# Kernel optimization log

Measured on AMD Instinct MI355X. Metric: run time of the kernel, lower is better.

Reference implementation:

```python
import jax, jax.numpy as jnp
import numpy as np

N = 100000
E = 3200000
IN_DIM = 256
HID = 64
NC = 32
K1 = 2  # conv1 propagation steps
EPS = 1e-5


def setup_inputs() -> dict:
    key = jax.random.key(0)
    ks = jax.random.split(key, 8)
    x = jax.random.normal(ks[0], (N, IN_DIM), dtype=jnp.float32)
    src = jax.random.randint(ks[1], (E,), 0, N)
    dst = jax.random.randint(ks[2], (E,), 0, N)
    W1 = jax.random.normal(ks[3], (IN_DIM, HID), dtype=jnp.float32) / np.sqrt(IN_DIM)
    b1 = jnp.zeros((HID,), dtype=jnp.float32)
    gamma = jnp.ones((HID,), dtype=jnp.float32)
    beta = jnp.zeros((HID,), dtype=jnp.float32)
    W2 = jax.random.normal(ks[4], (HID, NC), dtype=jnp.float32) / np.sqrt(HID)
    b2 = jnp.zeros((NC,), dtype=jnp.float32)
    return {"x": x, "src": src, "dst": dst, "W1": W1, "b1": b1,
            "gamma": gamma, "beta": beta, "W2": W2, "b2": b2}


def _gcn_norm(src, dst, n):
    # deg includes self loop (add_self_loops=True): deg[i] = 1 + in-degree
    deg = jax.ops.segment_sum(jnp.ones_like(src, dtype=jnp.float32), dst, num_segments=n) + 1.0
    dinv = jax.lax.rsqrt(deg)
    w_edge = dinv[src] * dinv[dst]      # [E] normalized edge weights
    w_self = dinv * dinv                # [N] self-loop weights (1/deg)
    return w_edge, w_self


def _propagate(h, src, dst, w_edge, w_self, n):
    # out = D^-1/2 (A+I) D^-1/2 h  via gather-scale-scatter
    msg = w_edge[:, None] * h[src]
    agg = jax.ops.segment_sum(msg, dst, num_segments=n)
    return agg + w_self[:, None] * h


def reference(x, src, dst, W1, b1, gamma, beta, W2, b2):
    n = x.shape[0]
    w_edge, w_self = _gcn_norm(src, dst, n)
    # conv1: K-step propagation then linear
    h = x
    for _ in range(K1):
        h = _propagate(h, src, dst, w_edge, w_self, n)
    h = h @ W1 + b1
    # batchnorm (training-mode batch stats over nodes, biased variance)
    mean = jnp.mean(h, axis=0)
    var = jnp.mean(jnp.square(h - mean), axis=0)
    h = (h - mean) * jax.lax.rsqrt(var + EPS) * gamma + beta
    h = jax.nn.selu(h)
    # dropout p=0.0 -> identity
    # conv2: 1-step propagation then linear
    h = _propagate(h, src, dst, w_edge, w_self, n)
    h = h @ W2 + b2
    return jax.nn.log_softmax(h, axis=1)
```

## Files before the change

kernel.cpp:

```cpp
#include <hip/hip_runtime.h>
#include <hip/hip_fp16.h>

#define NN 100000
#define EE 3200000
#define NB 256
#define NPB 391
#define BCAP 13568
#define NBLK_A 512
#define CHUNK_A (EE / NBLK_A)

#define OFF_AF   0UL
#define OFF_AH   25600000UL
#define OFF_BH   38400000UL
#define OFF_CNT  (OFF_BH + 65536UL)
#define OFF_LOC  (OFF_CNT + 524288UL)
#define OFF_P    (OFF_LOC + 524288UL)
#define OFF_CSR  51200000UL
#define OFF_RP   64000000UL
#define OFF_DINV 64400384UL
#define OFF_SEG  64800768UL
#define OFF_BASE 64808960UL
#define OFF_BN   64813056UL
#define OFF_SS   64813568UL

typedef __attribute__((ext_vector_type(8))) short bf16x8;
typedef __attribute__((ext_vector_type(4))) float f32x4;

__global__ __launch_bounds__(256) void passA2(const int* __restrict__ src, const int* __restrict__ dst,
                                              int* __restrict__ cnt, int* __restrict__ loc,
                                              unsigned* __restrict__ gbuf) {
    __shared__ unsigned ebuf[CHUNK_A];
    __shared__ int hist[NB], cur[NB], sc[NB];
    int t = threadIdx.x, b = blockIdx.x;
    hist[t] = 0;
    __syncthreads();
    int beg = b * CHUNK_A;
    for (int i = t; i < CHUNK_A; i += 256)
        atomicAdd(&hist[dst[beg + i] / NPB], 1);
    __syncthreads();
    int h = hist[t];
    sc[t] = h;
    __syncthreads();
    for (int off = 1; off < 256; off <<= 1) {
        int v = (t >= off) ? sc[t - off] : 0;
        __syncthreads();
        sc[t] += v;
        __syncthreads();
    }
    int ex = sc[t] - h;
    cur[t] = ex;
    loc[b * NB + t] = ex;
    cnt[b * NB + t] = h;
    __syncthreads();
    for (int i = t; i < CHUNK_A; i += 256) {
        int d = dst[beg + i];
        int k = d / NPB;
        int dl = d - k * NPB;
        int p = atomicAdd(&cur[k], 1);
        ebuf[p] = ((unsigned)dl << 17) | (unsigned)src[beg + i];
    }
    __syncthreads();
    for (int i = t; i < CHUNK_A; i += 256)
        gbuf[beg + i] = ebuf[i];
}

__global__ __launch_bounds__(512) void colscan(const int* __restrict__ cnt, int* __restrict__ P,
                                               int* __restrict__ total) {
    __shared__ int s[512];
    int k = blockIdx.x, t = threadIdx.x;
    int v = cnt[t * NB + k];
    s[t] = v;
    __syncthreads();
    for (int off = 1; off < 512; off <<= 1) {
        int u = (t >= off) ? s[t - off] : 0;
        __syncthreads();
        s[t] += u;
        __syncthreads();
    }
    P[t * NB + k] = s[t] - v;
    if (t == 511) total[k] = s[511];
}

__global__ __launch_bounds__(256) void basescan(const int* __restrict__ total, int* __restrict__ base,
                                                int* __restrict__ rp) {
    __shared__ int s[256];
    int t = threadIdx.x;
    int v = total[t];
    s[t] = v;
    __syncthreads();
    for (int off = 1; off < 256; off <<= 1) {
        int u = (t >= off) ? s[t - off] : 0;
        __syncthreads();
        s[t] += u;
        __syncthreads();
    }
    base[t] = s[t] - v;
    if (t == 255) { base[256] = s[255]; rp[NN] = s[255]; }
}

__global__ __launch_bounds__(512) void passB2(const unsigned* __restrict__ gbuf,
                                              const int* __restrict__ cnt, const int* __restrict__ loc,
                                              const int* __restrict__ P, const int* __restrict__ total,
                                              const int* __restrict__ base,
                                              int* __restrict__ rp, float* __restrict__ dinv,
                                              int* __restrict__ csr) {
    __shared__ unsigned ebuf[BCAP];
    __shared__ int deg_l[NPB];
    __shared__ int off_l[NPB];
    __shared__ int s[512];
    int k = blockIdx.x, t = threadIdx.x;
    int nb = min(total[k], BCAP);
    for (int i = t; i < NPB; i += 512) deg_l[i] = 0;
    int wid = t >> 6, lane = t & 63;
    for (int b = wid; b < NBLK_A; b += 8) {
        int n = cnt[b * NB + k];
        int so = b * CHUNK_A + loc[b * NB + k];
        int dofs = P[b * NB + k];
        for (int e = lane; e < n; e += 64)
            if (dofs + e < BCAP) ebuf[dofs + e] = gbuf[so + e];
    }
    __syncthreads();
    for (int j = t; j < nb; j += 512) atomicAdd(&deg_l[ebuf[j] >> 17], 1);
    __syncthreads();
    int d0 = (t < NPB) ? deg_l[t] : 0;
    s[t] = d0;
    __syncthreads();
    for (int off = 1; off < 512; off <<= 1) {
        int v = (t >= off) ? s[t - off] : 0;
        __syncthreads();
        s[t] += v;
        __syncthreads();
    }
    if (t < NPB) off_l[t] = s[t] - d0;
    __syncthreads();
    int nodebase = k * NPB;
    int cbase = base[k];
    for (int i = t; i < NPB; i += 512) {
        int node = nodebase + i;
        if (node < NN) {
            rp[node] = cbase + off_l[i];
            dinv[node] = rsqrtf((float)deg_l[i] + 1.0f);
        }
    }
    __syncthreads();
    for (int j = t; j < nb; j += 512) {
        unsigned e = ebuf[j];
        int p = atomicAdd(&off_l[e >> 17], 1);
        csr[cbase + p] = (int)(e & 0x1FFFFu);
    }
}

__global__ __launch_bounds__(256) void wprep(const float* __restrict__ W1, short* __restrict__ wf) {
    int e = blockIdx.x * 256 + threadIdx.x;
    if (e >= 16384) return;
    int j = e & 7, lane = (e >> 3) & 63, nt = (e >> 9) & 3, ks = e >> 11;
    int k = ks * 32 + (lane >> 4) * 8 + j;
    int col = nt * 16 + (lane & 15);
    float w = W1[k * 64 + col];
    unsigned b = __float_as_uint(w);
    short hi = (short)(b >> 16);
    float hf = __uint_as_float(b & 0xFFFF0000u);
    float lo = w - hf;
    short lov = (short)(__float_as_uint(lo) >> 16);
    wf[((size_t)(ks * 8 + nt * 2 + 0) * 64 + lane) * 8 + j] = hi;
    wf[((size_t)(ks * 8 + nt * 2 + 1) * 64 + lane) * 8 + j] = lov;
}

__global__ __launch_bounds__(256) void gemm1(const float* __restrict__ x, const short* __restrict__ wf,
                                             const float* __restrict__ dinv, __half* __restrict__ Ah) {
    int wid = threadIdx.x >> 6, lane = threadIdx.x & 63;
    int g = blockIdx.x * 4 + wid;
    if (g >= NN / 16) return;
    int lrow = g * 16 + (lane & 15);
    int kgrp = (lane >> 4) * 8;
    const float* xp = x + (size_t)lrow * 256 + kgrp;
    f32x4 acc[4];
    #pragma unroll
    for (int nt = 0; nt < 4; ++nt) acc[nt] = (f32x4){0.f, 0.f, 0.f, 0.f};
    for (int ks = 0; ks < 8; ++ks) {
        float4 f0 = *(const float4*)(xp + ks * 32);
        float4 f1 = *(const float4*)(xp + ks * 32 + 4);
        bf16x8 a_hi, a_lo;
        const float* fp = &f0.x;
        #pragma unroll
        for (int j = 0; j < 8; ++j) {
            float f = (j < 4) ? fp[j] : (&f1.x)[j - 4];
            unsigned b = __float_as_uint(f);
            a_hi[j] = (short)(b >> 16);
            float lo = f - __uint_as_float(b & 0xFFFF0000u);
            a_lo[j] = (short)(__float_as_uint(lo) >> 16);
        }
        const short* wfk = wf + (size_t)(ks * 8) * 64 * 8;
        #pragma unroll
        for (int nt = 0; nt < 4; ++nt) {
            bf16x8 b_hi = *(const bf16x8*)(wfk + ((nt * 2 + 0) * 64 + lane) * 8);
            bf16x8 b_lo = *(const bf16x8*)(wfk + ((nt * 2 + 1) * 64 + lane) * 8);
            acc[nt] = __builtin_amdgcn_mfma_f32_16x16x32_bf16(a_hi, b_hi, acc[nt], 0, 0, 0);
            acc[nt] = __builtin_amdgcn_mfma_f32_16x16x32_bf16(a_hi, b_lo, acc[nt], 0, 0, 0);
            acc[nt] = __builtin_amdgcn_mfma_f32_16x16x32_bf16(a_lo, b_hi, acc[nt], 0, 0, 0);
        }
    }
    int mb = (lane >> 4) * 4;
    #pragma unroll
    for (int reg = 0; reg < 4; ++reg) {
        int row = g * 16 + mb + reg;
        float dv = dinv[row];
        #pragma unroll
        for (int nt = 0; nt < 4; ++nt)
            Ah[(size_t)row * 64 + nt * 16 + (lane & 15)] = __float2half(acc[nt][reg] * dv);
    }
}

template <int P>
__global__ __launch_bounds__(256) void agg64h(const __half* __restrict__ h, __half* __restrict__ outp,
                                              const int* __restrict__ rp, const int* __restrict__ csr,
                                              const float* __restrict__ dinv) {
    int lane = threadIdx.x & 63;
    int node = (blockIdx.x << 2) + (threadIdx.x >> 6);
    if (node >= NN) return;
    int hid = lane >> 5;
    int c2 = (lane & 31) * 2;
    float dd = dinv[node];
    float ax = 0.f, ay = 0.f, bx = 0.f, by = 0.f;
    if (hid == 0) {
        __half2 sv = *(const __half2*)(h + (size_t)node * 64 + c2);
        ax = __half2float(sv.x); ay = __half2float(sv.y);
    }
    int beg = rp[node], end = rp[node + 1];
    for (int j0 = beg; j0 < end; j0 += 64) {
        int m = end - j0; if (m > 64) m = 64;
        int s = csr[j0 + (lane < m ? lane : 0)];
        int j = 0;
        for (; j + 15 < m; j += 16) {
            int i0 = __shfl(s, j + hid);
            int i1 = __shfl(s, j + 2 + hid);
            int i2 = __shfl(s, j + 4 + hid);
            int i3 = __shfl(s, j + 6 + hid);
            int i4 = __shfl(s, j + 8 + hid);
            int i5 = __shfl(s, j + 10 + hid);
            int i6 = __shfl(s, j + 12 + hid);
            int i7 = __shfl(s, j + 14 + hid);
            __half2 v0 = *(const __half2*)(h + (size_t)i0 * 64 + c2);
            __half2 v1 = *(const __half2*)(h + (size_t)i1 * 64 + c2);
            __half2 v2 = *(const __half2*)(h + (size_t)i2 * 64 + c2);
            __half2 v3 = *(const __half2*)(h + (size_t)i3 * 64 + c2);
            __half2 v4 = *(const __half2*)(h + (size_t)i4 * 64 + c2);
            __half2 v5 = *(const __half2*)(h + (size_t)i5 * 64 + c2);
            __half2 v6 = *(const __half2*)(h + (size_t)i6 * 64 + c2);
            __half2 v7 = *(const __half2*)(h + (size_t)i7 * 64 + c2);
            ax += __half2float(v0.x) + __half2float(v2.x);
            ay += __half2float(v0.y) + __half2float(v2.y);
            bx += __half2float(v1.x) + __half2float(v3.x);
            by += __half2float(v1.y) + __half2float(v3.y);
            ax += __half2float(v4.x) + __half2float(v6.x);
            ay += __half2float(v4.y) + __half2float(v6.y);
            bx += __half2float(v5.x) + __half2float(v7.x);
            by += __half2float(v5.y) + __half2float(v7.y);
        }
        for (; j + 7 < m; j += 8) {
            int i0 = __shfl(s, j + hid);
            int i1 = __shfl(s, j + 2 + hid);
            int i2 = __shfl(s, j + 4 + hid);
            int i3 = __shfl(s, j + 6 + hid);
            __half2 v0 = *(const __half2*)(h + (size_t)i0 * 64 + c2);
            __half2 v1 = *(const __half2*)(h + (size_t)i1 * 64 + c2);
            __half2 v2 = *(const __half2*)(h + (size_t)i2 * 64 + c2);
            __half2 v3 = *(const __half2*)(h + (size_t)i3 * 64 + c2);
            ax += __half2float(v0.x) + __half2float(v2.x);
            ay += __half2float(v0.y) + __half2float(v2.y);
            bx += __half2float(v1.x) + __half2float(v3.x);
            by += __half2float(v1.y) + __half2float(v3.y);
        }
        for (; j < m; j += 2) {
            int idx = j + hid;
            int cidx = idx < m ? idx : m - 1;
            int sj = __shfl(s, cidx);
            if (idx < m) {
                __half2 v = *(const __half2*)(h + (size_t)sj * 64 + c2);
                ax += __half2float(v.x); ay += __half2float(v.y);
            }
        }
    }
    float sx = ax + bx, sy = ay + by;
    sx += __shfl(sx, lane ^ 32);
    sy += __shfl(sy, lane ^ 32);
    if (hid == 0) {
        float w = (P == 2) ? dd * dd : dd;
        __half2 o;
        o.x = __float2half(sx * w); o.y = __float2half(sy * w);
        *(__half2*)(outp + (size_t)node * 64 + c2) = o;
    }
}

__global__ __launch_bounds__(256) void agg32f(const __half* __restrict__ U, float* __restrict__ outp,
                                              const int* __restrict__ rp, const int* __restrict__ csr,
                                              const float* __restrict__ dinv, const float* __restrict__ b2) {
    int lane = threadIdx.x & 63;
    int node = (blockIdx.x << 2) + (threadIdx.x >> 6);
    if (node >= NN) return;
    int gid = lane >> 4;
    int c2 = (lane & 15) * 2;
    float dd = dinv[node];
    float ax = 0.f, ay = 0.f;
    if (gid == 0) {
        __half2 sv = *(const __half2*)(U + (size_t)node * 32 + c2);
        ax = __half2float(sv.x); ay = __half2float(sv.y);
    }
    int beg = rp[node], end = rp[node + 1];
    for (int j0 = beg; j0 < end; j0 += 64) {
        int m = end - j0; if (m > 64) m = 64;
        int s = csr[j0 + (lane < m ? lane : 0)];
        int j = 0;
        for (; j + 15 < m; j += 16) {
            int i0 = __shfl(s, j + gid);
            int i1 = __shfl(s, j + 4 + gid);
            int i2 = __shfl(s, j + 8 + gid);
            int i3 = __shfl(s, j + 12 + gid);
            __half2 v0 = *(const __half2*)(U + (size_t)i0 * 32 + c2);
            __half2 v1 = *(const __half2*)(U + (size_t)i1 * 32 + c2);
            __half2 v2 = *(const __half2*)(U + (size_t)i2 * 32 + c2);
            __half2 v3 = *(const __half2*)(U + (size_t)i3 * 32 + c2);
            ax += __half2float(v0.x) + __half2float(v1.x) + __half2float(v2.x) + __half2float(v3.x);
            ay += __half2float(v0.y) + __half2float(v1.y) + __half2float(v2.y) + __half2float(v3.y);
        }
        for (; j + 7 < m; j += 8) {
            int i0 = __shfl(s, j + gid);
            int i1 = __shfl(s, j + 4 + gid);
            __half2 v0 = *(const __half2*)(U + (size_t)i0 * 32 + c2);
            __half2 v1 = *(const __half2*)(U + (size_t)i1 * 32 + c2);
            ax += __half2float(v0.x) + __half2float(v1.x);
            ay += __half2float(v0.y) + __half2float(v1.y);
        }
        for (; j < m; j += 4) {
            int idx = j + gid;
            int cidx = idx < m ? idx : m - 1;
            int sj = __shfl(s, cidx);
            if (idx < m) {
                __half2 v = *(const __half2*)(U + (size_t)sj * 32 + c2);
                ax += __half2float(v.x); ay += __half2float(v.y);
            }
        }
    }
    ax += __shfl(ax, lane ^ 16); ay += __shfl(ay, lane ^ 16);
    ax += __shfl(ax, lane ^ 32); ay += __shfl(ay, lane ^ 32);
    float v0 = ax * dd + b2[c2];
    float v1 = ay * dd + b2[c2 + 1];
    float mx = fmaxf(v0, v1);
    mx = fmaxf(mx, __shfl_xor(mx, 1));
    mx = fmaxf(mx, __shfl_xor(mx, 2));
    mx = fmaxf(mx, __shfl_xor(mx, 4));
    mx = fmaxf(mx, __shfl_xor(mx, 8));
    float sum = __expf(v0 - mx) + __expf(v1 - mx);
    sum += __shfl_xor(sum, 1);
    sum += __shfl_xor(sum, 2);
    sum += __shfl_xor(sum, 4);
    sum += __shfl_xor(sum, 8);
    if (gid == 0) {
        float ls = __logf(sum);
        *(float2*)(outp + (size_t)node * 32 + c2) = make_float2(v0 - mx - ls, v1 - mx - ls);
    }
}

__global__ __launch_bounds__(256) void bn_stats(const __half* __restrict__ A, float* __restrict__ bn) {
    int t = threadIdx.x;
    int c = t & 63, rg = t >> 6;
    float s = 0.f, sq = 0.f;
    for (int r = blockIdx.x * 4 + rg; r < NN; r += gridDim.x * 4) {
        float v = __half2float(A[(size_t)r * 64 + c]);
        s += v; sq += v * v;
    }
    __shared__ float ls[256], lq[256];
    ls[t] = s; lq[t] = sq;
    __syncthreads();
    if (t < 64) {
        float S = ls[t] + ls[t + 64] + ls[t + 128] + ls[t + 192];
        float Q = lq[t] + lq[t + 64] + lq[t + 128] + lq[t + 192];
        atomicAdd(&bn[t], S);
        atomicAdd(&bn[64 + t], Q);
    }
}

__global__ void bn_final(const float* __restrict__ bn, const float* __restrict__ gamma,
                         const float* __restrict__ beta, float* __restrict__ ss) {
    int c = threadIdx.x;
    float mean = bn[c] / (float)NN;
    float var = bn[64 + c] / (float)NN - mean * mean;
    float sc = gamma[c] * rsqrtf(var + 1e-5f);
    ss[c] = sc;
    ss[64 + c] = beta[c] - mean * sc;
}

__global__ __launch_bounds__(256) void gemm2(const __half* __restrict__ A, const float* __restrict__ W2,
                                             const float* __restrict__ ss, const float* __restrict__ dinv,
                                             __half* __restrict__ U) {
    __shared__ float w2s[64 * 32];
    __shared__ float sc[64], sh[64];
    for (int i = threadIdx.x; i < 512; i += 256)
        ((float4*)w2s)[i] = ((const float4*)W2)[i];
    if (threadIdx.x < 64) {
        sc[threadIdx.x] = ss[threadIdx.x];
        sh[threadIdx.x] = ss[64 + threadIdx.x];
    }
    __syncthreads();
    const float SELU_S = 1.0507009873554805f;
    const float SELU_AS = 1.7580993408473766f;
    int lane = threadIdx.x & 31, grp = threadIdx.x >> 5;
    int node = blockIdx.x * 8 + grp;
    if (node >= NN) return;
    const __half* Ar = A + (size_t)node * 64;
    float v0 = __half2float(Ar[lane]);
    float v1 = __half2float(Ar[lane + 32]);
    v0 = v0 * sc[lane] + sh[lane];
    v1 = v1 * sc[lane + 32] + sh[lane + 32];
    v0 = v0 > 0.f ? SELU_S * v0 : SELU_AS * (__expf(v0) - 1.0f);
    v1 = v1 > 0.f ? SELU_S * v1 : SELU_AS * (__expf(v1) - 1.0f);
    float acc = 0.f;
    #pragma unroll
    for (int j = 0; j < 32; ++j) {
        acc += __shfl(v0, j, 32) * w2s[j * 32 + lane];
        acc += __shfl(v1, j, 32) * w2s[(j + 32) * 32 + lane];
    }
    U[(size_t)node * 32 + lane] = __float2half(dinv[node] * acc);
}

extern "C" void kernel_launch(void* const* d_in, const int* in_sizes, int n_in,
                              void* d_out, int out_size, void* d_ws, size_t ws_size,
                              hipStream_t stream) {
    const float* x     = (const float*)d_in[0];
    const int*   src   = (const int*)d_in[1];
    const int*   dst   = (const int*)d_in[2];
    const float* W1    = (const float*)d_in[3];
    const float* gamma = (const float*)d_in[5];
    const float* beta  = (const float*)d_in[6];
    const float* W2    = (const float*)d_in[7];
    const float* b2    = (const float*)d_in[8];
    float* out = (float*)d_out;

    char* ws = (char*)d_ws;
    __half*   Af   = (__half*)(ws + OFF_AF);
    unsigned* gbuf = (unsigned*)(ws + OFF_AF);
    __half*   Ah   = (__half*)(ws + OFF_AH);
    __half*   Bh   = (__half*)(ws + OFF_BH);
    short*    wf   = (short*)(ws + OFF_BH);
    __half*   Uh   = (__half*)(ws + OFF_BH);
    int*      cnt  = (int*)(ws + OFF_CNT);
    int*      loc  = (int*)(ws + OFF_LOC);
    int*      Pm   = (int*)(ws + OFF_P);
    int*      csr  = (int*)(ws + OFF_CSR);
    int*      rp   = (int*)(ws + OFF_RP);
    float*    dinv = (float*)(ws + OFF_DINV);
    int*      tot  = (int*)(ws + OFF_SEG);
    int*      base = (int*)(ws + OFF_BASE);
    float*    bn   = (float*)(ws + OFF_BN);
    float*    ssb  = (float*)(ws + OFF_SS);

    hipMemsetAsync(bn, 0, 128 * sizeof(float), stream);

    wprep<<<64, 256, 0, stream>>>(W1, wf);

    passA2<<<NBLK_A, 256, 0, stream>>>(src, dst, cnt, loc, gbuf);
    colscan<<<NB, 512, 0, stream>>>(cnt, Pm, tot);
    basescan<<<1, 256, 0, stream>>>(tot, base, rp);
    passB2<<<NB, 512, 0, stream>>>(gbuf, cnt, loc, Pm, tot, base, rp, dinv, csr);

    gemm1<<<(NN / 16 + 3) / 4, 256, 0, stream>>>(x, wf, dinv, Ah);
    agg64h<2><<<NN / 4, 256, 0, stream>>>(Ah, Bh, rp, csr, dinv);
    agg64h<1><<<NN / 4, 256, 0, stream>>>(Bh, Af, rp, csr, dinv);

    bn_stats<<<1024, 256, 0, stream>>>(Af, bn);
    bn_final<<<1, 64, 0, stream>>>(bn, gamma, beta, ssb);

    gemm2<<<NN / 8, 256, 0, stream>>>(Af, W2, ssb, dinv, Uh);
    agg32f<<<NN / 4, 256, 0, stream>>>(Uh, out, rp, csr, dinv, b2);
}
```

Before: 388.7 us.

## Drop column scan and LDS staging in CSR build; read gbuf per-thread directly

Removes the colscan kernel and computes per-bucket totals inside basescan by summing 512 counts per thread. passB2 no longer stages bucket edges into shared memory; each of the 512 threads walks its own source block's segment of gbuf serially, twice (degree count, then scatter). This saves a launch and the LDS capacity limit, but basescan becomes a long serial loop in a single block, and the per-thread serial reads of gbuf are uncoalesced and read twice.

```diff
diff --git a/kernel.cpp b/kernel.cpp
--- a/kernel.cpp
+++ b/kernel.cpp
@@ -5,7 +5,6 @@
 #define EE 3200000
 #define NB 256
 #define NPB 391
-#define BCAP 13568
 #define NBLK_A 512
 #define CHUNK_A (EE / NBLK_A)
 
@@ -14,11 +13,9 @@
 #define OFF_BH   38400000UL
 #define OFF_CNT  (OFF_BH + 65536UL)
 #define OFF_LOC  (OFF_CNT + 524288UL)
-#define OFF_P    (OFF_LOC + 524288UL)
 #define OFF_CSR  51200000UL
 #define OFF_RP   64000000UL
 #define OFF_DINV 64400384UL
-#define OFF_SEG  64800768UL
 #define OFF_BASE 64808960UL
 #define OFF_BN   64813056UL
 #define OFF_SS   64813568UL
@@ -64,28 +61,12 @@
         gbuf[beg + i] = ebuf[i];
 }
 
-__global__ __launch_bounds__(512) void colscan(const int* __restrict__ cnt, int* __restrict__ P,
-                                               int* __restrict__ total) {
-    __shared__ int s[512];
-    int k = blockIdx.x, t = threadIdx.x;
-    int v = cnt[t * NB + k];
-    s[t] = v;
-    __syncthreads();
-    for (int off = 1; off < 512; off <<= 1) {
-        int u = (t >= off) ? s[t - off] : 0;
-        __syncthreads();
-        s[t] += u;
-        __syncthreads();
-    }
-    P[t * NB + k] = s[t] - v;
-    if (t == 511) total[k] = s[511];
-}
-
-__global__ __launch_bounds__(256) void basescan(const int* __restrict__ total, int* __restrict__ base,
+__global__ __launch_bounds__(256) void basescan(const int* __restrict__ cnt, int* __restrict__ base,
                                                 int* __restrict__ rp) {
     __shared__ int s[256];
     int t = threadIdx.x;
-    int v = total[t];
+    int v = 0;
+    for (int b = 0; b < NBLK_A; ++b) v += cnt[b * NB + t];
     s[t] = v;
     __syncthreads();
     for (int off = 1; off < 256; off <<= 1) {
@@ -100,27 +81,19 @@
 
 __global__ __launch_bounds__(512) void passB2(const unsigned* __restrict__ gbuf,
                                               const int* __restrict__ cnt, const int* __restrict__ loc,
-                                              const int* __restrict__ P, const int* __restrict__ total,
                                               const int* __restrict__ base,
                                               int* __restrict__ rp, float* __restrict__ dinv,
                                               int* __restrict__ csr) {
-    __shared__ unsigned ebuf[BCAP];
     __shared__ int deg_l[NPB];
     __shared__ int off_l[NPB];
     __shared__ int s[512];
     int k = blockIdx.x, t = threadIdx.x;
-    int nb = min(total[k], BCAP);
     for (int i = t; i < NPB; i += 512) deg_l[i] = 0;
-    int wid = t >> 6, lane = t & 63;
-    for (int b = wid; b < NBLK_A; b += 8) {
-        int n = cnt[b * NB + k];
-        int so = b * CHUNK_A + loc[b * NB + k];
-        int dofs = P[b * NB + k];
-        for (int e = lane; e < n; e += 64)
-            if (dofs + e < BCAP) ebuf[dofs + e] = gbuf[so + e];
-    }
-    __syncthreads();
-    for (int j = t; j < nb; j += 512) atomicAdd(&deg_l[ebuf[j] >> 17], 1);
+    __syncthreads();
+    int n  = cnt[t * NB + k];
+    int so = t * CHUNK_A + loc[t * NB + k];
+    for (int e = 0; e < n; ++e)
+        atomicAdd(&deg_l[gbuf[so + e] >> 17], 1);
     __syncthreads();
     int d0 = (t < NPB) ? deg_l[t] : 0;
     s[t] = d0;
@@ -143,10 +116,10 @@
         }
     }
     __syncthreads();
-    for (int j = t; j < nb; j += 512) {
-        unsigned e = ebuf[j];
-        int p = atomicAdd(&off_l[e >> 17], 1);
-        csr[cbase + p] = (int)(e & 0x1FFFFu);
+    for (int e = 0; e < n; ++e) {
+        unsigned v = gbuf[so + e];
+        int p = atomicAdd(&off_l[v >> 17], 1);
+        csr[cbase + p] = (int)(v & 0x1FFFFu);
     }
 }
 
@@ -445,11 +418,9 @@
     __half*   Uh   = (__half*)(ws + OFF_BH);
     int*      cnt  = (int*)(ws + OFF_CNT);
     int*      loc  = (int*)(ws + OFF_LOC);
-    int*      Pm   = (int*)(ws + OFF_P);
     int*      csr  = (int*)(ws + OFF_CSR);
     int*      rp   = (int*)(ws + OFF_RP);
     float*    dinv = (float*)(ws + OFF_DINV);
-    int*      tot  = (int*)(ws + OFF_SEG);
     int*      base = (int*)(ws + OFF_BASE);
     float*    bn   = (float*)(ws + OFF_BN);
     float*    ssb  = (float*)(ws + OFF_SS);
@@ -459,9 +430,8 @@
     wprep<<<64, 256, 0, stream>>>(W1, wf);
 
     passA2<<<NBLK_A, 256, 0, stream>>>(src, dst, cnt, loc, gbuf);
-    colscan<<<NB, 512, 0, stream>>>(cnt, Pm, tot);
-    basescan<<<1, 256, 0, stream>>>(tot, base, rp);
-    passB2<<<NB, 512, 0, stream>>>(gbuf, cnt, loc, Pm, tot, base, rp, dinv, csr);
+    basescan<<<1, 256, 0, stream>>>(cnt, base, rp);
+    passB2<<<NB, 512, 0, stream>>>(gbuf, cnt, loc, base, rp, dinv, csr);
 
     gemm1<<<(NN / 16 + 3) / 4, 256, 0, stream>>>(x, wf, dinv, Ah);
     agg64h<2><<<NN / 4, 256, 0, stream>>>(Ah, Bh, rp, csr, dinv);
```

Measured after the change: 354.5 us. 8.8% less time.
